# Kernel optimization log

Hardware: AMD Instinct MI355X
Metric: run time of the kernel (lower is better)

Reference implementation:

```python
import jax, jax.numpy as jnp
import numpy as np

C = 256
G = 32            # GroupNorm groups = min(32, C)
DQK = C // 8      # q/k channel dim
EPS = 1e-5


def setup_inputs() -> dict:
    key = jax.random.key(0)
    ks = jax.random.split(key, 10)
    B, H, W = 4, 64, 64
    s = 0.02
    return {
        "x": jax.random.normal(ks[0], (B, C, H, W), dtype=jnp.float32),
        "gamma": jnp.ones((C,), jnp.float32),
        "beta": jnp.zeros((C,), jnp.float32),
        "wq": jax.random.normal(ks[1], (DQK, C), jnp.float32) * s,
        "bq": jnp.zeros((DQK,), jnp.float32),
        "wk": jax.random.normal(ks[2], (DQK, C), jnp.float32) * s,
        "bk": jnp.zeros((DQK,), jnp.float32),
        "wv": jax.random.normal(ks[3], (C, C), jnp.float32) * s,
        "bv": jnp.zeros((C,), jnp.float32),
        "wp": jax.random.normal(ks[4], (C, C), jnp.float32) * s,
        "bp": jnpp if False else jnp.zeros((C,), jnp.float32),
    }


def reference(x, gamma, beta, wq, bq, wk, bk, wv, bv, wp, bp):
    B, Cc, H, W = x.shape
    N = H * W
    # GroupNorm(32, C), affine
    h = x.reshape(B, G, Cc // G, H, W)
    mu = h.mean(axis=(2, 3, 4), keepdims=True)
    var = h.var(axis=(2, 3, 4), keepdims=True)
    h = (h - mu) * jax.lax.rsqrt(var + EPS)
    h = h.reshape(B, Cc, N) * gamma[:, None] + beta[:, None]
    # 1x1 convs == per-token linear maps over channels
    q = jnp.einsum('dc,bcn->bnd', wq, h) + bq            # [B, N, DQK]
    k = jnp.einsum('dc,bcn->bdn', wk, h) + bk[:, None]   # [B, DQK, N]
    v = jnp.einsum('ec,bcn->ben', wv, h) + bv[:, None]   # [B, C, N]
    scale = DQK ** (-0.5)
    attn = jax.nn.softmax(jnp.einsum('bnd,bdm->bnm', q, k) * scale, axis=-1)
    out = jnp.einsum('bnm,bem->ben', attn, v)            # [B, C, N]
    proj = jnp.einsum('fe,ben->bfn', wp, out) + bp[:, None]
    return x + proj.reshape(B, Cc, H, W)
```

## Files before the change

kernel.cpp:

```cpp
#include <hip/hip_runtime.h>
#include <hip/hip_bf16.h>

#define NB 4
#define CD 256
#define NT 4096
#define DQ 32

typedef __attribute__((ext_vector_type(8))) __bf16 bf16x8;
typedef __attribute__((ext_vector_type(16))) float float16v;
typedef __attribute__((ext_vector_type(4))) unsigned int uint4v;
typedef __attribute__((ext_vector_type(2))) unsigned int uint2v;

#if __has_builtin(__builtin_amdgcn_exp2f)
#define EXP2(x) __builtin_amdgcn_exp2f(x)
#else
#define EXP2(x) exp2f(x)
#endif

__device__ inline unsigned short f2bf(float f) {
  unsigned u = __float_as_uint(f);
  u += 0x7fffu + ((u >> 16) & 1u);
  return (unsigned short)(u >> 16);
}

#define BARRIER() asm volatile("s_waitcnt lgkmcnt(0)\n\ts_barrier" ::: "memory")

__global__ __launch_bounds__(256) void gn_prep(
    const float* __restrict__ x, float* __restrict__ accum,
    const float* __restrict__ wq, const float* __restrict__ wk,
    const float* __restrict__ wv, const float* __restrict__ wp,
    const float* __restrict__ bq, const float* __restrict__ bk,
    const float* __restrict__ bv, unsigned short* __restrict__ wqkv,
    unsigned short* __restrict__ wpb, float* __restrict__ bias) {
  int bx = blockIdx.x;
  int tid = threadIdx.x;
  if (bx < 512) {
    int bg = bx >> 2, ch = bx & 3;
    const float4* xp = (const float4*)(x + (size_t)bg * 32768 + ch * 8192);
    float s = 0.f, ss = 0.f;
#pragma unroll
    for (int i = 0; i < 8; i++) {
      float4 v = xp[tid + 256 * i];
      s += v.x + v.y + v.z + v.w;
      ss += v.x * v.x + v.y * v.y + v.z * v.z + v.w * v.w;
    }
    int wid = tid >> 6, lane = tid & 63;
#pragma unroll
    for (int off = 32; off >= 1; off >>= 1) {
      s += __shfl_xor(s, off);
      ss += __shfl_xor(ss, off);
    }
    __shared__ float red[8];
    if (lane == 0) { red[wid] = s; red[4 + wid] = ss; }
    __syncthreads();
    if (tid == 0) {
      accum[2 * bx] = red[0] + red[1] + red[2] + red[3];
      accum[2 * bx + 1] = red[4] + red[5] + red[6] + red[7];
    }
  } else {
    const float scale2 = 0.2550348909867343f;
    int i = (bx - 512) * 256 + tid;
    if (i < 320 * 256) {
      int j = i >> 8, c = i & 255;
      float v;
      if (j < 32) v = wq[j * 256 + c] * scale2;
      else if (j < 64) v = wk[(j - 32) * 256 + c];
      else v = wv[(j - 64) * 256 + c];
      wqkv[i] = f2bf(v);
    } else if (i < 320 * 256 + 256 * 256) {
      int k = i - 320 * 256;
      wpb[k] = f2bf(wp[k]);
    } else if (i < 320 * 256 + 256 * 256 + 320) {
      int j = i - (320 * 256 + 256 * 256);
      float v;
      if (j < 32) v = bq[j] * scale2;
      else if (j < 64) v = bk[j - 32];
      else v = bv[j - 64];
      bias[j] = v;
    }
  }
}

__global__ __launch_bounds__(256) void gn_apply(
    const float* __restrict__ x, const float* __restrict__ gamma,
    const float* __restrict__ beta, const float* __restrict__ accum,
    unsigned short* __restrict__ h) {
  int bg = blockIdx.x >> 2, nc = blockIdx.x & 3;
  int tid = threadIdx.x;
  float S = accum[8 * bg] + accum[8 * bg + 2] + accum[8 * bg + 4] +
            accum[8 * bg + 6];
  float SS = accum[8 * bg + 1] + accum[8 * bg + 3] + accum[8 * bg + 5] +
             accum[8 * bg + 7];
  float mu = S * (1.f / 32768.f);
  float var = SS * (1.f / 32768.f) - mu * mu;
  float rstd = rsqrtf(var + 1e-5f);
  int b = bg >> 5, g = bg & 31, c0 = g * 8;
  float gam[8], bet[8];
#pragma unroll
  for (int j = 0; j < 8; j++) { gam[j] = gamma[c0 + j]; bet[j] = beta[c0 + j]; }
  const float* xb = x + (size_t)bg * 32768;
#pragma unroll
  for (int i = 0; i < 4; i++) {
    int n = nc * 1024 + tid + 256 * i;
    unsigned short hv[8];
#pragma unroll
    for (int j = 0; j < 8; j++) {
      float y = (xb[j * NT + n] - mu) * rstd * gam[j] + bet[j];
      hv[j] = f2bf(y);
    }
    *(uint4v*)(h + ((size_t)(b * NT + n) * CD + c0)) = *(uint4v*)hv;
  }
}

__global__ __launch_bounds__(256) void qkv_gemm(
    const unsigned short* __restrict__ A, const unsigned short* __restrict__ H,
    const float* __restrict__ bias, unsigned short* __restrict__ qk,
    unsigned short* __restrict__ v) {
  int nt = blockIdx.x, mt = blockIdx.y, b = blockIdx.z;
  int tid = threadIdx.x, lane = tid & 63;
  int w = tid >> 6, mi = w & 1, ni = w >> 1;
  int l31 = lane & 31, hh = lane >> 5;
  int m_base = mt * 64 + 32 * mi;
  int n_base = nt * 128 + 64 * ni;
  const unsigned short* Arow = A + (size_t)(m_base + l31) * 256 + 8 * hh;
  const unsigned short* Hb = H + (size_t)b * NT * CD;
  const unsigned short* h0 = Hb + (size_t)(n_base + l31) * CD + 8 * hh;
  const unsigned short* h1 = h0 + (size_t)32 * CD;
  float16v acc0, acc1;
#pragma unroll
  for (int r = 0; r < 16; r++) { acc0[r] = 0.f; acc1[r] = 0.f; }
#pragma unroll
  for (int s = 0; s < 16; s++) {
    bf16x8 af = *(const bf16x8*)(Arow + 16 * s);
    bf16x8 b0 = *(const bf16x8*)(h0 + 16 * s);
    bf16x8 b1 = *(const bf16x8*)(h1 + 16 * s);
    acc0 = __builtin_amdgcn_mfma_f32_32x32x16_bf16(af, b0, acc0, 0, 0, 0);
    acc1 = __builtin_amdgcn_mfma_f32_32x32x16_bf16(af, b1, acc1, 0, 0, 0);
  }
  float bj[16];
  int jr[16];
#pragma unroll
  for (int r = 0; r < 16; r++) {
    jr[r] = m_base + (r & 3) + 8 * (r >> 2) + 4 * hh;
    bj[r] = bias[jr[r]];
  }
#pragma unroll
  for (int half = 0; half < 2; half++) {
    int n = n_base + 32 * half + l31;
#pragma unroll
    for (int r = 0; r < 16; r++) {
      float val = (half ? acc1[r] : acc0[r]) + bj[r];
      int j = jr[r];
      if (j < 64) {
        qk[((size_t)b * NT + n) * 64 + j] = f2bf(val);
      } else {
        int e = j - 64;
        int itg = n >> 6, sp = (n >> 4) & 3;
        int ls = ((n >> 3) & 1) * 32 + (e & 31);
        int el = n & 7, et = e >> 5;
        v[((((size_t)b * 64 + itg) * 8 + et) * 4 + sp) * 512 + ls * 8 + el] =
            f2bf(val);
      }
    }
  }
}

#define K_STAGE(PCUR)                                                         \
  if (tid >= 256) {                                                           \
    *(uint4v*)&Ks[(((PCUR) + 1) & 1) * 2304 + skr * 36 + skc] = kreg;         \
    int pk_ = (PCUR) + 2 <= 31 ? (PCUR) + 2 : 31;                             \
    kreg =                                                                    \
        *(const uint4v*)&qkb[(size_t)(mbase + pk_ * 64 + skr) * 64 + 32 + skc]; \
  }

#define QK_STEP(PCUR)                                                         \
  if (w < 4) {                                                                \
    float16v st;                                                              \
    _Pragma("unroll") for (int r = 0; r < 16; r++) st[r] = 0.f;               \
    _Pragma("unroll") for (int s = 0; s < 2; s++) {                           \
      bf16x8 af = *(const bf16x8*)&Ks[((PCUR) & 1) * 2304 +                   \
                                      (32 * ks2 + l31) * 36 + 16 * s + 8 * hh]; \
      st = __builtin_amdgcn_mfma_f32_32x32x16_bf16(af, qfr[s], st, 0, 0, 0);  \
    }                                                                         \
    _Pragma("unroll") for (int rq = 0; rq < 4; rq++) {                        \
      float e0 = EXP2(st[4 * rq + 0]);                                        \
      float e1 = EXP2(st[4 * rq + 1]);                                        \
      float e2 = EXP2(st[4 * rq + 2]);                                        \
      float e3 = EXP2(st[4 * rq + 3]);                                        \
      lsum += (e0 + e1) + (e2 + e3);                                          \
      uint2v pw;                                                              \
      pw[0] = __builtin_amdgcn_perm(__float_as_uint(e1), __float_as_uint(e0), \
                                    0x07060302u);                             \
      pw[1] = __builtin_amdgcn_perm(__float_as_uint(e3), __float_as_uint(e2), \
                                    0x07060302u);                             \
      *(uint2v*)&Pbuf[((PCUR) & 1) * 4352 + (qs * 32 + l31) * 68 + 8 * rq +   \
                      4 * hh + 32 * ks2] = pw;                                \
    }                                                                         \
  }

#define PV_STEP(PPREV, CURV)                                                  \
  {                                                                           \
    _Pragma("unroll") for (int sp = 0; sp < 4; sp++) {                        \
      bf16x8 a0 = *(const bf16x8*)&Pbuf[((PPREV) & 1) * 4352 + l31 * 68 +     \
                                        16 * sp + 8 * hh];                    \
      bf16x8 a1 = *(const bf16x8*)&Pbuf[((PPREV) & 1) * 4352 +                \
                                        (32 + l31) * 68 + 16 * sp + 8 * hh];  \
      acc[0] = __builtin_amdgcn_mfma_f32_32x32x16_bf16(a0, CURV[sp], acc[0],  \
                                                       0, 0, 0);              \
      acc[1] = __builtin_amdgcn_mfma_f32_32x32x16_bf16(a1, CURV[sp], acc[1],  \
                                                       0, 0, 0);              \
    }                                                                         \
  }

#define V_LOAD(DST, ITX)                                                      \
  {                                                                           \
    const unsigned short* vp_ = vbase + (size_t)(ITX)*16384;                  \
    _Pragma("unroll") for (int u = 0; u < 4; u++)                             \
        DST[u] = *(const bf16x8*)(vp_ + u * 512);                             \
  }

__global__ __launch_bounds__(512, 4) void attn_fused(
    const unsigned short* __restrict__ qk, const unsigned short* __restrict__ Vp,
    unsigned short* __restrict__ Pa, unsigned short* __restrict__ Pb,
    float* __restrict__ lp4) {
  int L = blockIdx.x;
  int xv = L & 7;
  int b = xv >> 1;
  int kh = xv & 1;
  int n0 = (L >> 3) * 64;
  int tid = threadIdx.x, lane = tid & 63, w = tid >> 6;
  int l31 = lane & 31, hh = lane >> 5;
  int qs = w & 1, ks2 = (w >> 1) & 1;

  __shared__ unsigned short Ks[2 * 2304];
  __shared__ unsigned short Pbuf[2 * 4352];

  const unsigned short* qkb = qk + (size_t)b * NT * 64;
  const unsigned short* vit = Vp + ((size_t)b * 64 + kh * 32) * 16384;
  const unsigned short* vbase = vit + (size_t)w * 4 * 512 + lane * 8;

  bf16x8 qfr[2];
  if (w < 4) {
    int n_g = n0 + 32 * qs + l31;
    qfr[0] = *(const bf16x8*)&qkb[(size_t)n_g * 64 + 8 * hh];
    qfr[1] = *(const bf16x8*)&qkb[(size_t)n_g * 64 + 8 * hh + 16];
  }

  int tK = tid - 256;
  int skr = tK >> 2, skc = (tK & 3) * 8;
  int mbase = kh * 2048;
  uint4v kreg;

  float16v acc[2];
#pragma unroll
  for (int q2 = 0; q2 < 2; q2++)
#pragma unroll
    for (int r = 0; r < 16; r++) acc[q2][r] = 0.f;
  float lsum = 0.f;

  bf16x8 vA[4], vB[4];
  V_LOAD(vA, 0);
  if (tid >= 256) {
    kreg = *(const uint4v*)&qkb[(size_t)(mbase + skr) * 64 + 32 + skc];
    *(uint4v*)&Ks[skr * 36 + skc] = kreg;
    kreg = *(const uint4v*)&qkb[(size_t)(mbase + 64 + skr) * 64 + 32 + skc];
  }
  BARRIER();

  K_STAGE(0);
  QK_STEP(0);
  V_LOAD(vB, 1);
  BARRIER();

  for (int p = 1; p < 31; p += 2) {
    K_STAGE(p);
    QK_STEP(p);
    PV_STEP(p - 1, vA);
    V_LOAD(vA, p + 1);
    BARRIER();
    K_STAGE(p + 1);
    QK_STEP(p + 1);
    PV_STEP(p, vB);
    V_LOAD(vB, p + 2);
    BARRIER();
  }
  QK_STEP(31);
  PV_STEP(30, vA);
  BARRIER();
  PV_STEP(31, vB);

  if (w < 4) {
    lsum += __shfl_xor(lsum, 32);
    if (hh == 0) {
      lp4[(size_t)((kh * 2 + ks2) * NB + b) * NT + n0 + 32 * qs + l31] = lsum;
    }
  }

  unsigned short* Pout = (kh ? Pb : Pa) + (size_t)b * NT * CD;
#pragma unroll
  for (int r = 0; r < 16; r++) {
    int nl = (r & 3) + 8 * (r >> 2) + 4 * hh;
    Pout[(size_t)(n0 + nl) * CD + 32 * w + l31] = f2bf(acc[0][r]);
    Pout[(size_t)(n0 + 32 + nl) * CD + 32 * w + l31] = f2bf(acc[1][r]);
  }
}

__device__ inline bf16x8 combine_frag(const unsigned short* p0,
                                      const unsigned short* p1, float inv) {
  uint4v ua = *(const uint4v*)p0;
  uint4v ub = *(const uint4v*)p1;
  uint4v r;
#pragma unroll
  for (int j = 0; j < 4; j++) {
    float lo = __uint_as_float(ua[j] << 16) + __uint_as_float(ub[j] << 16);
    float hi = __uint_as_float(ua[j] & 0xffff0000u) +
               __uint_as_float(ub[j] & 0xffff0000u);
    lo *= inv;
    hi *= inv;
    r[j] = __builtin_amdgcn_perm(__float_as_uint(hi), __float_as_uint(lo),
                                 0x07060302u);
  }
  return *(bf16x8*)&r;
}

__global__ __launch_bounds__(256) void proj_gemm(
    const unsigned short* __restrict__ Wp, const unsigned short* __restrict__ Pa,
    const unsigned short* __restrict__ Pb, const float* __restrict__ lp4,
    const float* __restrict__ bp, const float* __restrict__ x,
    float* __restrict__ out) {
  int nt = blockIdx.x, mt = blockIdx.y, b = blockIdx.z;
  int tid = threadIdx.x, lane = tid & 63;
  int w = tid >> 6, mi = w & 1, ni = w >> 1;
  int l31 = lane & 31, hh = lane >> 5;
  int m_base = mt * 64 + 32 * mi;
  int n_base = nt * 128 + 64 * ni;
  const unsigned short* Arow = Wp + (size_t)(m_base + l31) * 256 + 8 * hh;
  int nA = n_base + l31, nB = nA + 32;
  float lA = 0.f, lB = 0.f;
#pragma unroll
  for (int s4 = 0; s4 < 4; s4++) {
    lA += lp4[(size_t)(s4 * NB + b) * NT + nA];
    lB += lp4[(size_t)(s4 * NB + b) * NT + nB];
  }
  float invA = 1.f / lA, invB = 1.f / lB;
  const unsigned short* a0 = Pa + ((size_t)b * NT + nA) * CD + 8 * hh;
  const unsigned short* a1 = Pa + ((size_t)b * NT + nB) * CD + 8 * hh;
  const unsigned short* c0 = Pb + ((size_t)b * NT + nA) * CD + 8 * hh;
  const unsigned short* c1 = Pb + ((size_t)b * NT + nB) * CD + 8 * hh;
  float16v acc0, acc1;
#pragma unroll
  for (int r = 0; r < 16; r++) { acc0[r] = 0.f; acc1[r] = 0.f; }
#pragma unroll
  for (int s = 0; s < 16; s++) {
    bf16x8 af = *(const bf16x8*)(Arow + 16 * s);
    bf16x8 b0 = combine_frag(a0 + 16 * s, c0 + 16 * s, invA);
    bf16x8 b1 = combine_frag(a1 + 16 * s, c1 + 16 * s, invB);
    acc0 = __builtin_amdgcn_mfma_f32_32x32x16_bf16(af, b0, acc0, 0, 0, 0);
    acc1 = __builtin_amdgcn_mfma_f32_32x32x16_bf16(af, b1, acc1, 0, 0, 0);
  }
#pragma unroll
  for (int half = 0; half < 2; half++) {
    int n = n_base + 32 * half + l31;
#pragma unroll
    for (int r = 0; r < 16; r++) {
      int f = m_base + (r & 3) + 8 * (r >> 2) + 4 * hh;
      size_t idx = ((size_t)b * CD + f) * NT + n;
      out[idx] = x[idx] + (half ? acc1[r] : acc0[r]) + bp[f];
    }
  }
}

extern "C" void kernel_launch(void* const* d_in, const int* in_sizes, int n_in,
                              void* d_out, int out_size, void* d_ws,
                              size_t ws_size, hipStream_t stream) {
  (void)in_sizes; (void)n_in; (void)out_size; (void)ws_size;
  const float* x = (const float*)d_in[0];
  const float* gamma = (const float*)d_in[1];
  const float* beta = (const float*)d_in[2];
  const float* wq = (const float*)d_in[3];
  const float* bq = (const float*)d_in[4];
  const float* wk = (const float*)d_in[5];
  const float* bk = (const float*)d_in[6];
  const float* wv = (const float*)d_in[7];
  const float* bv = (const float*)d_in[8];
  const float* wp = (const float*)d_in[9];
  const float* bp = (const float*)d_in[10];
  float* out = (float*)d_out;

  char* ws = (char*)d_ws;
  unsigned short* h_ws = (unsigned short*)ws;
  unsigned short* qk_ws = (unsigned short*)(ws + 8388608);
  unsigned short* v_ws = (unsigned short*)(ws + 10485760);
  unsigned short* o_ws = (unsigned short*)(ws + 18874368);
  unsigned short* wqkv_b = (unsigned short*)(ws + 27262976);
  unsigned short* wp_b = (unsigned short*)(ws + 27426816);
  float* bias_q = (float*)(ws + 27557888);
  float* accum = (float*)(ws + 27559168);
  float* lp4 = (float*)(ws + 27563264);

  gn_prep<<<1090, 256, 0, stream>>>(x, accum, wq, wk, wv, wp, bq, bk, bv,
                                    wqkv_b, wp_b, bias_q);
  gn_apply<<<512, 256, 0, stream>>>(x, gamma, beta, accum, h_ws);
  dim3 gq(32, 5, NB);
  qkv_gemm<<<gq, 256, 0, stream>>>(wqkv_b, h_ws, bias_q, qk_ws, v_ws);
  attn_fused<<<512, 512, 0, stream>>>(qk_ws, v_ws, h_ws, o_ws, lp4);
  dim3 gp(32, 4, NB);
  proj_gemm<<<gp, 256, 0, stream>>>(wp_b, h_ws, o_ws, lp4, bp, x, out);
}
```

Before: 186.1 us.

## Fuse GroupNorm stats and apply into one kernel; raise MFMA wave priority

Combines the GroupNorm statistics pass and the normalize pass into a single kernel where one 1024-thread block handles a whole (batch, group), keeping x in registers so it is read from memory only once. This removes one kernel launch and the second read of x, but uses only 128 blocks for the normalize work, so fewer workgroups share that part. Separately, the attention kernel raises wave priority around its MFMA sections with s_setprio, so matrix work is favored over other waves.

```diff
diff --git a/kernel.cpp b/kernel.cpp
--- a/kernel.cpp
+++ b/kernel.cpp
@@ -25,41 +25,70 @@
 
 #define BARRIER() asm volatile("s_waitcnt lgkmcnt(0)\n\ts_barrier" ::: "memory")
 
-__global__ __launch_bounds__(256) void gn_prep(
-    const float* __restrict__ x, float* __restrict__ accum,
-    const float* __restrict__ wq, const float* __restrict__ wk,
-    const float* __restrict__ wv, const float* __restrict__ wp,
-    const float* __restrict__ bq, const float* __restrict__ bk,
-    const float* __restrict__ bv, unsigned short* __restrict__ wqkv,
+__global__ __launch_bounds__(1024) void gn_fused(
+    const float* __restrict__ x, const float* __restrict__ gamma,
+    const float* __restrict__ beta, const float* __restrict__ wq,
+    const float* __restrict__ wk, const float* __restrict__ wv,
+    const float* __restrict__ wp, const float* __restrict__ bq,
+    const float* __restrict__ bk, const float* __restrict__ bv,
+    unsigned short* __restrict__ h, unsigned short* __restrict__ wqkv,
     unsigned short* __restrict__ wpb, float* __restrict__ bias) {
   int bx = blockIdx.x;
   int tid = threadIdx.x;
-  if (bx < 512) {
-    int bg = bx >> 2, ch = bx & 3;
-    const float4* xp = (const float4*)(x + (size_t)bg * 32768 + ch * 8192);
+  if (bx < 128) {
+    int b = bx >> 5, g = bx & 31, c0 = g * 8;
+    const float4* xp = (const float4*)(x + (size_t)bx * 32768);
+    float va[32];
     float s = 0.f, ss = 0.f;
 #pragma unroll
     for (int i = 0; i < 8; i++) {
-      float4 v = xp[tid + 256 * i];
-      s += v.x + v.y + v.z + v.w;
-      ss += v.x * v.x + v.y * v.y + v.z * v.z + v.w * v.w;
-    }
-    int wid = tid >> 6, lane = tid & 63;
+      float4 t4 = xp[i * 1024 + tid];
+      va[4 * i + 0] = t4.x;
+      va[4 * i + 1] = t4.y;
+      va[4 * i + 2] = t4.z;
+      va[4 * i + 3] = t4.w;
+      s += t4.x + t4.y + t4.z + t4.w;
+      ss += t4.x * t4.x + t4.y * t4.y + t4.z * t4.z + t4.w * t4.w;
+    }
 #pragma unroll
     for (int off = 32; off >= 1; off >>= 1) {
       s += __shfl_xor(s, off);
       ss += __shfl_xor(ss, off);
     }
-    __shared__ float red[8];
-    if (lane == 0) { red[wid] = s; red[4 + wid] = ss; }
+    __shared__ float red[32];
+    int wid = tid >> 6;
+    if ((tid & 63) == 0) {
+      red[wid] = s;
+      red[16 + wid] = ss;
+    }
     __syncthreads();
-    if (tid == 0) {
-      accum[2 * bx] = red[0] + red[1] + red[2] + red[3];
-      accum[2 * bx + 1] = red[4] + red[5] + red[6] + red[7];
+    float S = 0.f, SS = 0.f;
+#pragma unroll
+    for (int i = 0; i < 16; i++) {
+      S += red[i];
+      SS += red[16 + i];
+    }
+    float mu = S * (1.f / 32768.f);
+    float rstd = rsqrtf(SS * (1.f / 32768.f) - mu * mu + 1e-5f);
+    float gam[8], bet[8];
+#pragma unroll
+    for (int i = 0; i < 8; i++) {
+      gam[i] = gamma[c0 + i] * rstd;
+      bet[i] = beta[c0 + i] - mu * gamma[c0 + i] * rstd;
+    }
+    unsigned short* hb = h + (size_t)b * NT * CD + c0;
+#pragma unroll
+    for (int j = 0; j < 4; j++) {
+      unsigned short hv[8];
+#pragma unroll
+      for (int i = 0; i < 8; i++) {
+        hv[i] = f2bf(va[4 * i + j] * gam[i] + bet[i]);
+      }
+      *(uint4v*)(hb + (size_t)(4 * tid + j) * CD) = *(uint4v*)hv;
     }
   } else {
     const float scale2 = 0.2550348909867343f;
-    int i = (bx - 512) * 256 + tid;
+    int i = (bx - 128) * 1024 + tid;
     if (i < 320 * 256) {
       int j = i >> 8, c = i & 255;
       float v;
@@ -81,37 +110,6 @@
   }
 }
 
-__global__ __launch_bounds__(256) void gn_apply(
-    const float* __restrict__ x, const float* __restrict__ gamma,
-    const float* __restrict__ beta, const float* __restrict__ accum,
-    unsigned short* __restrict__ h) {
-  int bg = blockIdx.x >> 2, nc = blockIdx.x & 3;
-  int tid = threadIdx.x;
-  float S = accum[8 * bg] + accum[8 * bg + 2] + accum[8 * bg + 4] +
-            accum[8 * bg + 6];
-  float SS = accum[8 * bg + 1] + accum[8 * bg + 3] + accum[8 * bg + 5] +
-             accum[8 * bg + 7];
-  float mu = S * (1.f / 32768.f);
-  float var = SS * (1.f / 32768.f) - mu * mu;
-  float rstd = rsqrtf(var + 1e-5f);
-  int b = bg >> 5, g = bg & 31, c0 = g * 8;
-  float gam[8], bet[8];
-#pragma unroll
-  for (int j = 0; j < 8; j++) { gam[j] = gamma[c0 + j]; bet[j] = beta[c0 + j]; }
-  const float* xb = x + (size_t)bg * 32768;
-#pragma unroll
-  for (int i = 0; i < 4; i++) {
-    int n = nc * 1024 + tid + 256 * i;
-    unsigned short hv[8];
-#pragma unroll
-    for (int j = 0; j < 8; j++) {
-      float y = (xb[j * NT + n] - mu) * rstd * gam[j] + bet[j];
-      hv[j] = f2bf(y);
-    }
-    *(uint4v*)(h + ((size_t)(b * NT + n) * CD + c0)) = *(uint4v*)hv;
-  }
-}
-
 __global__ __launch_bounds__(256) void qkv_gemm(
     const unsigned short* __restrict__ A, const unsigned short* __restrict__ H,
     const float* __restrict__ bias, unsigned short* __restrict__ qk,
@@ -177,11 +175,13 @@
   if (w < 4) {                                                                \
     float16v st;                                                              \
     _Pragma("unroll") for (int r = 0; r < 16; r++) st[r] = 0.f;               \
+    __builtin_amdgcn_s_setprio(1);                                            \
     _Pragma("unroll") for (int s = 0; s < 2; s++) {                           \
       bf16x8 af = *(const bf16x8*)&Ks[((PCUR) & 1) * 2304 +                   \
                                       (32 * ks2 + l31) * 36 + 16 * s + 8 * hh]; \
       st = __builtin_amdgcn_mfma_f32_32x32x16_bf16(af, qfr[s], st, 0, 0, 0);  \
     }                                                                         \
+    __builtin_amdgcn_s_setprio(0);                                            \
     _Pragma("unroll") for (int rq = 0; rq < 4; rq++) {                        \
       float e0 = EXP2(st[4 * rq + 0]);                                        \
       float e1 = EXP2(st[4 * rq + 1]);                                        \
@@ -200,6 +200,7 @@
 
 #define PV_STEP(PPREV, CURV)                                                  \
   {                                                                           \
+    __builtin_amdgcn_s_setprio(1);                                            \
     _Pragma("unroll") for (int sp = 0; sp < 4; sp++) {                        \
       bf16x8 a0 = *(const bf16x8*)&Pbuf[((PPREV) & 1) * 4352 + l31 * 68 +     \
                                         16 * sp + 8 * hh];                    \
@@ -210,6 +211,7 @@
       acc[1] = __builtin_amdgcn_mfma_f32_32x32x16_bf16(a1, CURV[sp], acc[1],  \
                                                        0, 0, 0);              \
     }                                                                         \
+    __builtin_amdgcn_s_setprio(0);                                            \
   }
 
 #define V_LOAD(DST, ITX)                                                      \
@@ -395,12 +397,10 @@
   unsigned short* wqkv_b = (unsigned short*)(ws + 27262976);
   unsigned short* wp_b = (unsigned short*)(ws + 27426816);
   float* bias_q = (float*)(ws + 27557888);
-  float* accum = (float*)(ws + 27559168);
   float* lp4 = (float*)(ws + 27563264);
 
-  gn_prep<<<1090, 256, 0, stream>>>(x, accum, wq, wk, wv, wp, bq, bk, bv,
-                                    wqkv_b, wp_b, bias_q);
-  gn_apply<<<512, 256, 0, stream>>>(x, gamma, beta, accum, h_ws);
+  gn_fused<<<273, 1024, 0, stream>>>(x, gamma, beta, wq, wk, wv, wp, bq, bk,
+                                     bv, h_ws, wqkv_b, wp_b, bias_q);
   dim3 gq(32, 5, NB);
   qkv_gemm<<<gq, 256, 0, stream>>>(wqkv_b, h_ws, bias_q, qk_ws, v_ws);
   attn_fused<<<512, 512, 0, stream>>>(qk_ws, v_ws, h_ws, o_ws, lp4);
```

Result: no change. 185.7 us (-0.2%).
